# Optimization experiments

Measured on AMD Instinct MI355X. Metric: run time of the kernel, lower is better.

## Reference

```python
import jax, jax.numpy as jnp
import numpy as np

NUM_CLASSES = 10
HIDDEN = 64
_LABEL2MASK_THRESHOL = 500


def setup_inputs() -> dict:
    key = jax.random.key(0)
    ks = jax.random.split(key, 5)
    B, h, w = 4, 60, 80
    feature1 = jax.random.normal(ks[0], (B, 512, h, w), jnp.float32)
    feature2 = jax.random.normal(ks[1], (B, 512, h // 2, w // 2), jnp.float32)
    # kaiming_normal (fan_in, relu): std = sqrt(2 / fan_in)
    w1 = jax.random.normal(ks[2], (HIDDEN, 512), jnp.float32) * np.sqrt(2.0 / 512)
    w2 = jax.random.normal(ks[3], (HIDDEN, 512), jnp.float32) * np.sqrt(2.0 / 512)
    wc = jax.random.normal(ks[4], (NUM_CLASSES + 1, HIDDEN), jnp.float32) * np.sqrt(2.0 / HIDDEN)
    b1 = jnp.zeros((HIDDEN,), jnp.float32)
    b2 = jnp.zeros((HIDDEN,), jnp.float32)
    bc = jnp.zeros((NUM_CLASSES + 1,), jnp.float32)
    return {"feature1": feature1, "feature2": feature2, "w1": w1, "b1": b1,
            "w2": w2, "b2": b2, "wc": wc, "bc": bc}


def _conv1x1(x, w, b):
    # x: (B,C,H,W), w: (O,C), b: (O,)
    return jnp.einsum('bchw,oc->bohw', x, w) + b[None, :, None, None]


def _resize2x(x, s):
    B, C, H, W = x.shape
    # torch nn.Upsample(mode='bilinear', align_corners=False) == half-pixel bilinear
    return jax.image.resize(x, (B, C, H * s, W * s), method='bilinear')


def _label2bbx(seg, num_classes, thresh):
    # seg: (B,H,W) int. Fixed-shape, fully vectorized version of the nested
    # python-loop bbox extraction. Rows with pixel count < thresh are -1.
    B, H, W = seg.shape
    cls = jnp.arange(1, num_classes, dtype=seg.dtype)        # skip background cls 0
    mask = seg[:, None, :, :] == cls[None, :, None, None]    # (B,K,H,W)
    cnt = mask.sum(axis=(2, 3))
    xs = jnp.arange(W, dtype=jnp.int32)[None, None, None, :]
    ys = jnp.arange(H, dtype=jnp.int32)[None, None, :, None]
    x1 = jnp.min(jnp.where(mask, xs, W), axis=(2, 3))
    x2 = jnp.max(jnp.where(mask, xs, -1), axis=(2, 3))
    y1 = jnp.min(jnp.where(mask, ys, H), axis=(2, 3))
    y2 = jnp.max(jnp.where(mask, ys, -1), axis=(2, 3))
    K = num_classes - 1
    bid = jnp.broadcast_to(jnp.arange(B, dtype=jnp.int32)[:, None], (B, K))
    cid = jnp.broadcast_to(cls.astype(jnp.int32)[None, :], (B, K))
    rows = jnp.stack([bid, x1.astype(jnp.int32), y1.astype(jnp.int32),
                      x2.astype(jnp.int32), y2.astype(jnp.int32), cid], axis=-1)  # (B,K,6)
    valid = (cnt >= thresh)[..., None]
    rows = jnp.where(valid, rows, -1)
    return rows.reshape(B * K, 6)


def reference(feature1, feature2, w1, b1, w2, b2, wc, bc):
    f1 = jax.nn.relu(_conv1x1(feature1, w1, b1))
    f2 = jax.nn.relu(_conv1x1(feature2, w2, b2))
    f2 = _resize2x(f2, 2)
    feat = _resize2x(f1 + f2, 8)              # (B,64,480,640)
    logits = _conv1x1(feat, wc, bc)           # (B,11,480,640)
    probability = jax.nn.softmax(logits, axis=1)
    segmentation = jnp.argmax(probability, axis=1)
    bbx = _label2bbx(segmentation, NUM_CLASSES, _LABEL2MASK_THRESHOL)
    return probability, segmentation, bbx
```

## Files before the change

kernel.cpp:

```cpp
#include <hip/hip_runtime.h>

#define BN 4
#define CIN 512
#define H1 60
#define W1 80
#define P1 4800
#define H2 30
#define W2 40
#define P2 1200
#define HID 64
#define NCLS 11
#define HF 480
#define WF 640
#define PF 307200
#define THRESH 500

#define WT1_OFF 0
#define WT2_OFF 32768
#define F2_OFF  65536
#define PART_OFF F2_OFF
#define L_OFF   (65536 + 307200)
#define PP_OFF  603136

__device__ __forceinline__ void dma16(const float* g, float* l) {
    __builtin_amdgcn_global_load_lds(
        (const __attribute__((address_space(1))) void*)g,
        (__attribute__((address_space(3))) void*)l, 16, 0, 0);
}

__global__ void k0_init(const float* __restrict__ w1, const float* __restrict__ w2,
                        float* __restrict__ ws) {
    int idx = blockIdx.x * 256 + threadIdx.x;
    if (idx < 32768) {
        int c = idx >> 6, o = idx & 63;
        ws[WT1_OFF + idx] = w1[o * CIN + c];
    } else {
        int j = idx - 32768;
        int c = j >> 6, o = j & 63;
        ws[WT2_OFF + j] = w2[o * CIN + c];
    }
}

__global__ __launch_bounds__(256, 4) void k1_conv2(const float* __restrict__ x,
                                                   const float* __restrict__ b2,
                                                   float* __restrict__ ws) {
    __shared__ float lds[8320];
    const float* wt = ws + WT2_OFF;
    float* f2o = ws + F2_OFF;
    int blk = blockIdx.x;
    int b = blk / 150, tile = blk % 150;
    int t = threadIdx.x;
    int l = t & 63, w = t >> 6;
    int q = t & 1, og = (t >> 1) & 7, ch = t >> 4;
    int o0 = og * 8;
    int p0 = tile * 8;
    const float* xb = x + (size_t)b * CIN * P2 + p0;

    auto stage = [&](int s) {
        int buf = s & 1;
#pragma unroll
        for (int j = 0; j < 2; ++j) {
            int r0 = j * 128 + w * 32;
            int r  = r0 + (l >> 1);
            int cg = (r >> 4) * 32 + s * 16 + (r & 15);
            dma16(xb + (size_t)cg * P2 + (l & 1) * 4,
                  lds + buf * 2048 + r0 * 8);
        }
    };

    float acc[4][8];
#pragma unroll
    for (int j = 0; j < 4; ++j)
#pragma unroll
        for (int i = 0; i < 8; ++i) acc[j][i] = 0.f;

    stage(0);
    __syncthreads();
    const float* wp = wt + (ch * 32) * HID + o0;
    for (int s = 0; s < 2; ++s) {
        if (s < 1) stage(s + 1);
        const float* xs = lds + (s & 1) * 2048 + ch * 128 + q * 4;
#pragma unroll 4
        for (int cc = 0; cc < 16; ++cc) {
            float4 xv = *(const float4*)(xs + cc * 8);
            const float* wr = wp + (s * 16 + cc) * HID;
            float4 wa = *(const float4*)(wr);
            float4 wb = *(const float4*)(wr + 4);
            float w8[8] = {wa.x, wa.y, wa.z, wa.w, wb.x, wb.y, wb.z, wb.w};
            float x4[4] = {xv.x, xv.y, xv.z, xv.w};
#pragma unroll
            for (int j = 0; j < 4; ++j)
#pragma unroll
                for (int i = 0; i < 8; ++i) acc[j][i] = fmaf(w8[i], x4[j], acc[j][i]);
        }
        __syncthreads();
    }
#pragma unroll
    for (int j = 0; j < 4; ++j)
#pragma unroll
        for (int i = 0; i < 8; ++i)
            lds[ch * 520 + (q * 4 + j) * 65 + o0 + i] = acc[j][i];
    __syncthreads();

    if (t < 64) {
        int px = t >> 3, oo = (t & 7) * 8;
        float v[8];
#pragma unroll
        for (int i = 0; i < 8; ++i) {
            float s = 0.f;
#pragma unroll
            for (int c = 0; c < 16; ++c) s += lds[c * 520 + px * 65 + oo + i];
            v[i] = fmaxf(s + b2[oo + i], 0.f);
        }
        float* outp = f2o + ((size_t)b * P2 + p0 + px) * HID + oo;
        *(float4*)outp = make_float4(v[0], v[1], v[2], v[3]);
        *(float4*)(outp + 4) = make_float4(v[4], v[5], v[6], v[7]);
    }
}

__global__ __launch_bounds__(256, 2) void k2a_conv1(const float* __restrict__ x,
                                                    float* __restrict__ ws) {
    __shared__ float lds[16384];
    const float* wtg = ws + WT1_OFF;
    float* pp = ws + PP_OFF;
    int blk = blockIdx.x;
    int b = blk / 300;
    int rem = blk - b * 300;
    int hb = rem / 150;
    int tile = rem - hb * 150;
    int t = threadIdx.x;
    int l = t & 63;
    int q = t & 7, og = (t >> 3) & 7, ch = t >> 6;
    int o0 = og * 8;
    int p0 = tile * 32;
    const float* xc = x + (size_t)b * CIN * P1 + (size_t)(hb * 256 + ch * 64) * P1
                    + p0 + q * 4;

    float4 xA[8], xB[8];
    auto loadg = [&](float4* xb, int g) {
        const float* p = xc + (size_t)g * (8 * P1);
#pragma unroll
        for (int i = 0; i < 8; ++i) xb[i] = *(const float4*)(p + (size_t)i * P1);
    };

    loadg(xA, 0);

    {
        const float* src = wtg + hb * 16384 + ch * 4096;
#pragma unroll
        for (int i = 0; i < 16; ++i)
            dma16(src + i * 256 + l * 4, lds + ch * 4096 + i * 256);
    }
    __syncthreads();

    float acc[4][8];
#pragma unroll
    for (int j = 0; j < 4; ++j)
#pragma unroll
        for (int i = 0; i < 8; ++i) acc[j][i] = 0.f;

    const float* wl = lds + ch * 4096 + o0;
    auto computeg = [&](const float4* xb, int g) {
        const float* wr0 = wl + g * 8 * 64;
#pragma unroll
        for (int i = 0; i < 8; ++i) {
            float4 wa  = *(const float4*)(wr0 + i * 64);
            float4 wb4 = *(const float4*)(wr0 + i * 64 + 4);
            float w8[8] = {wa.x, wa.y, wa.z, wa.w, wb4.x, wb4.y, wb4.z, wb4.w};
            float x4[4] = {xb[i].x, xb[i].y, xb[i].z, xb[i].w};
#pragma unroll
            for (int j = 0; j < 4; ++j)
#pragma unroll
                for (int i2 = 0; i2 < 8; ++i2) acc[j][i2] = fmaf(w8[i2], x4[j], acc[j][i2]);
        }
    };

#pragma unroll 1
    for (int g = 0; g < 8; g += 2) {
        loadg(xB, min(g + 1, 7));
        computeg(xA, g);
        loadg(xA, min(g + 2, 7));
        computeg(xB, g + 1);
    }

    __syncthreads();
#pragma unroll
    for (int j = 0; j < 4; ++j)
#pragma unroll
        for (int i = 0; i < 8; ++i)
            lds[ch * 2080 + (q * 4 + j) * 65 + o0 + i] = acc[j][i];
    __syncthreads();

    {
        int px = t >> 3;
        int oo = (t & 7) * 8;
        float v[8];
#pragma unroll
        for (int i = 0; i < 8; ++i) {
            int a = px * 65 + oo + i;
            v[i] = lds[a] + lds[2080 + a] + lds[2 * 2080 + a] + lds[3 * 2080 + a];
        }
        float* outp = pp + ((size_t)(b * 2 + hb) * P1 + p0 + px) * HID + oo;
        *(float4*)outp = make_float4(v[0], v[1], v[2], v[3]);
        *(float4*)(outp + 4) = make_float4(v[4], v[5], v[6], v[7]);
    }
}

__global__ __launch_bounds__(256) void k2b_reduce(const float* __restrict__ b1,
                                                  const float* __restrict__ wc,
                                                  const float* __restrict__ bc,
                                                  float* __restrict__ ws) {
    __shared__ float g[2080];
    const float* pp = ws + PP_OFF;
    const float* f2 = ws + F2_OFF;
    float* lout = ws + L_OFF;
    int blk = blockIdx.x;
    int b = blk / 150, tile = blk % 150;
    int t = threadIdx.x;
    int p0 = tile * 32;

    {
        int px = t >> 3;
        int oo = (t & 7) * 8;
        int p = p0 + px;
        const float* h0 = pp + ((size_t)(b * 2 + 0) * P1 + p) * HID + oo;
        const float* h1 = pp + ((size_t)(b * 2 + 1) * P1 + p) * HID + oo;
        float4 a0 = *(const float4*)h0;
        float4 a1 = *(const float4*)(h0 + 4);
        float4 c0 = *(const float4*)h1;
        float4 c1 = *(const float4*)(h1 + 4);
        float hs[8] = {a0.x + c0.x, a0.y + c0.y, a0.z + c0.z, a0.w + c0.w,
                       a1.x + c1.x, a1.y + c1.y, a1.z + c1.z, a1.w + c1.w};

        int y = p / W1, xq = p - y * W1;
        float sy = fmaf((float)y, 0.5f, -0.25f);
        float fy = floorf(sy);
        float ty = sy - fy;
        int y0 = max(0, min(H2 - 1, (int)fy));
        int y1 = max(0, min(H2 - 1, (int)fy + 1));
        float sx = fmaf((float)xq, 0.5f, -0.25f);
        float fx = floorf(sx);
        float tx = sx - fx;
        int x0 = max(0, min(W2 - 1, (int)fx));
        int x1 = max(0, min(W2 - 1, (int)fx + 1));
        float wy0 = 1.f - ty, wx0 = 1.f - tx;
        const float* f2b = f2 + (size_t)b * P2 * HID;
        const float* r00 = f2b + (y0 * W2 + x0) * HID + oo;
        const float* r01 = f2b + (y0 * W2 + x1) * HID + oo;
        const float* r10 = f2b + (y1 * W2 + x0) * HID + oo;
        const float* r11 = f2b + (y1 * W2 + x1) * HID + oo;
#pragma unroll
        for (int i = 0; i < 8; ++i) {
            float f1v = fmaxf(hs[i] + b1[oo + i], 0.f);
            float v0 = r00[i] * wx0 + r01[i] * tx;
            float v1 = r10[i] * wx0 + r11[i] * tx;
            g[px * 65 + oo + i] = f1v + (v0 * wy0 + v1 * ty);
        }
    }
    __syncthreads();

    {
        int px2 = t & 31;
        int kg = t >> 5;
        int k2i = (kg < 3) ? kg + 8 : 8;
        float l1 = bc[kg];
        float l2 = bc[k2i];
#pragma unroll 8
        for (int o = 0; o < HID; ++o) {
            float gv = g[px2 * 65 + o];
            l1 = fmaf(wc[kg * HID + o], gv, l1);
            l2 = fmaf(wc[k2i * HID + o], gv, l2);
        }
        float* lrow = lout + ((size_t)b * P1 + p0 + px2) * 12;
        lrow[kg] = l1;
        if (kg < 3) lrow[kg + 8] = l2;
        else if (kg == 3) lrow[11] = 0.f;
    }
}

__global__ __launch_bounds__(256) void k4_main(float* __restrict__ out,
                                               float* __restrict__ ws) {
    __shared__ int s_cnt[9], s_x0[9], s_y0[9], s_x1[9], s_y1[9];
    const float* l = ws + L_OFF;
    int* partb = (int*)(ws + PART_OFF);
    int t = threadIdx.x;
    if (t < 9) { s_cnt[t] = 0; s_x0[t] = WF; s_y0[t] = HF; s_x1[t] = -1; s_y1[t] = -1; }
    __syncthreads();

    int fl = blockIdx.x * 256 + t;
    int b = fl / PF;
    int r = fl - b * PF;
    int Y = r / WF;
    int X = r - Y * WF;

    float sy = fmaf((float)Y, 0.125f, -0.4375f);
    float fy = floorf(sy);
    float ty = sy - fy;
    int y0 = max(0, min(H1 - 1, (int)fy));
    int y1 = max(0, min(H1 - 1, (int)fy + 1));
    float sx = fmaf((float)X, 0.125f, -0.4375f);
    float fx = floorf(sx);
    float tx = sx - fx;
    int x0 = max(0, min(W1 - 1, (int)fx));
    int x1 = max(0, min(W1 - 1, (int)fx + 1));
    float wy0 = 1.f - ty, wx0 = 1.f - tx;

    const float* lb = l + (size_t)b * P1 * 12;
    const float4* q00 = (const float4*)(lb + (y0 * W1 + x0) * 12);
    const float4* q01 = (const float4*)(lb + (y0 * W1 + x1) * 12);
    const float4* q10 = (const float4*)(lb + (y1 * W1 + x0) * 12);
    const float4* q11 = (const float4*)(lb + (y1 * W1 + x1) * 12);
    float l00[12], l01[12], l10[12], l11[12];
#pragma unroll
    for (int j = 0; j < 3; ++j) {
        ((float4*)l00)[j] = q00[j];
        ((float4*)l01)[j] = q01[j];
        ((float4*)l10)[j] = q10[j];
        ((float4*)l11)[j] = q11[j];
    }
    float li[11];
#pragma unroll
    for (int k = 0; k < 11; ++k) {
        float v0 = l00[k] * wx0 + l01[k] * tx;
        float v1 = l10[k] * wx0 + l11[k] * tx;
        li[k] = v0 * wy0 + v1 * ty;
    }
    int am = 0;
    float bm = li[0];
#pragma unroll
    for (int k = 1; k < 11; ++k) {
        if (li[k] > bm) { bm = li[k]; am = k; }
    }
    float e[11];
    float s = 0.f;
#pragma unroll
    for (int k = 0; k < 11; ++k) { e[k] = __expf(li[k] - bm); s += e[k]; }
    float rs = 1.f / s;
    size_t ob = (size_t)b * NCLS * PF + r;
#pragma unroll
    for (int k = 0; k < 11; ++k) out[ob + (size_t)k * PF] = e[k] * rs;
    out[(size_t)BN * NCLS * PF + fl] = (float)am;

    int lane = t & 63;
    int X0 = X & ~63;
    for (int c = 1; c <= 9; ++c) {
        unsigned long long m = __ballot(am == c);
        if (m != 0ULL && lane == 0) {
            int ci = c - 1;
            atomicAdd(&s_cnt[ci], (int)__popcll(m));
            atomicMin(&s_x0[ci], X0 + __builtin_ctzll(m));
            atomicMax(&s_x1[ci], X0 + 63 - __builtin_clzll(m));
            atomicMin(&s_y0[ci], Y);
            atomicMax(&s_y1[ci], Y);
        }
    }
    __syncthreads();
    if (t < 9) {
        int* pr = partb + blockIdx.x * 45 + t * 5;
        pr[0] = s_cnt[t];
        pr[1] = s_x0[t];
        pr[2] = s_y0[t];
        pr[3] = s_x1[t];
        pr[4] = s_y1[t];
    }
}

__global__ void k5_bbx(float* __restrict__ out, const float* __restrict__ ws) {
    const int* partb = (const int*)(ws + PART_OFF);
    int b = blockIdx.x / 9, c = blockIdx.x % 9;
    int t = threadIdx.x;
    int cnt = 0, mnx = WF, mny = HF, mxx = -1, mxy = -1;
    for (int i = t; i < 1200; i += 64) {
        const int* pr = partb + (size_t)(b * 1200 + i) * 45 + c * 5;
        cnt += pr[0];
        mnx = min(mnx, pr[1]);
        mny = min(mny, pr[2]);
        mxx = max(mxx, pr[3]);
        mxy = max(mxy, pr[4]);
    }
    for (int sft = 32; sft; sft >>= 1) {
        cnt += __shfl_xor(cnt, sft);
        mnx = min(mnx, __shfl_xor(mnx, sft));
        mny = min(mny, __shfl_xor(mny, sft));
        mxx = max(mxx, __shfl_xor(mxx, sft));
        mxy = max(mxy, __shfl_xor(mxy, sft));
    }
    if (t == 0) {
        float* row = out + (size_t)BN * NCLS * PF + (size_t)BN * PF + (size_t)(b * 9 + c) * 6;
        bool ok = cnt >= THRESH;
        row[0] = ok ? (float)b : -1.f;
        row[1] = ok ? (float)mnx : -1.f;
        row[2] = ok ? (float)mny : -1.f;
        row[3] = ok ? (float)mxx : -1.f;
        row[4] = ok ? (float)mxy : -1.f;
        row[5] = ok ? (float)(c + 1) : -1.f;
    }
}

extern "C" void kernel_launch(void* const* d_in, const int* in_sizes, int n_in,
                              void* d_out, int out_size, void* d_ws, size_t ws_size,
                              hipStream_t stream) {
    const float* f1 = (const float*)d_in[0];
    const float* f2 = (const float*)d_in[1];
    const float* w1 = (const float*)d_in[2];
    const float* b1 = (const float*)d_in[3];
    const float* w2 = (const float*)d_in[4];
    const float* b2 = (const float*)d_in[5];
    const float* wc = (const float*)d_in[6];
    const float* bc = (const float*)d_in[7];
    float* out = (float*)d_out;
    float* ws = (float*)d_ws;

    k0_init<<<dim3(256), dim3(256), 0, stream>>>(w1, w2, ws);
    k1_conv2<<<dim3(600), dim3(256), 0, stream>>>(f2, b2, ws);
    k2a_conv1<<<dim3(1200), dim3(256), 0, stream>>>(f1, ws);
    k2b_reduce<<<dim3(600), dim3(256), 0, stream>>>(b1, wc, bc, ws);
    k4_main<<<dim3(4800), dim3(256), 0, stream>>>(out, ws);
    k5_bbx<<<dim3(36), dim3(64), 0, stream>>>(out, ws);
}
```

Baseline: 167.3 us.

## Stage low-res logit rows in LDS per output row and add sched barriers

The upsample/softmax kernel now runs one 640-thread block per output row. It stages the two needed low-res logit rows into shared memory and reads the bilinear corners from LDS rather than from scattered global loads, so per-block partial bbox records drop from 1200 to 480 per image and the reduction kernel is adjusted to match. Separately, sched_barrier calls are inserted in the conv1 kernel to keep its load/compute software pipeline ordered. The price is a larger block, which can limit occupancy, plus an extra sync per block.

```diff
diff --git a/kernel.cpp b/kernel.cpp
--- a/kernel.cpp
+++ b/kernel.cpp
@@ -144,6 +144,7 @@
     };
 
     loadg(xA, 0);
+    __builtin_amdgcn_sched_barrier(0);
 
     {
         const float* src = wtg + hb * 16384 + ch * 4096;
@@ -178,8 +179,10 @@
 #pragma unroll 1
     for (int g = 0; g < 8; g += 2) {
         loadg(xB, min(g + 1, 7));
+        __builtin_amdgcn_sched_barrier(0);
         computeg(xA, g);
         loadg(xA, min(g + 2, 7));
+        __builtin_amdgcn_sched_barrier(0);
         computeg(xB, g + 1);
     }
 
@@ -278,38 +281,45 @@
     }
 }
 
-__global__ __launch_bounds__(256) void k4_main(float* __restrict__ out,
+__global__ __launch_bounds__(640) void k4_main(float* __restrict__ out,
                                                float* __restrict__ ws) {
+    __shared__ float sl[1920];
     __shared__ int s_cnt[9], s_x0[9], s_y0[9], s_x1[9], s_y1[9];
     const float* l = ws + L_OFF;
     int* partb = (int*)(ws + PART_OFF);
     int t = threadIdx.x;
     if (t < 9) { s_cnt[t] = 0; s_x0[t] = WF; s_y0[t] = HF; s_x1[t] = -1; s_y1[t] = -1; }
-    __syncthreads();
-
-    int fl = blockIdx.x * 256 + t;
-    int b = fl / PF;
-    int r = fl - b * PF;
-    int Y = r / WF;
-    int X = r - Y * WF;
+
+    int blk = blockIdx.x;
+    int b = blk / HF;
+    int Y = blk - b * HF;
 
     float sy = fmaf((float)Y, 0.125f, -0.4375f);
     float fy = floorf(sy);
     float ty = sy - fy;
     int y0 = max(0, min(H1 - 1, (int)fy));
     int y1 = max(0, min(H1 - 1, (int)fy + 1));
+    float wy0 = 1.f - ty;
+
+    const float* lb = l + (size_t)b * P1 * 12;
+    const float* row0 = lb + y0 * W1 * 12;
+    const float* row1 = lb + y1 * W1 * 12;
+    for (int i = t; i < 960; i += 640) sl[i] = row0[i];
+    for (int i = t; i < 960; i += 640) sl[960 + i] = row1[i];
+    __syncthreads();
+
+    int X = t;
     float sx = fmaf((float)X, 0.125f, -0.4375f);
     float fx = floorf(sx);
     float tx = sx - fx;
     int x0 = max(0, min(W1 - 1, (int)fx));
     int x1 = max(0, min(W1 - 1, (int)fx + 1));
-    float wy0 = 1.f - ty, wx0 = 1.f - tx;
-
-    const float* lb = l + (size_t)b * P1 * 12;
-    const float4* q00 = (const float4*)(lb + (y0 * W1 + x0) * 12);
-    const float4* q01 = (const float4*)(lb + (y0 * W1 + x1) * 12);
-    const float4* q10 = (const float4*)(lb + (y1 * W1 + x0) * 12);
-    const float4* q11 = (const float4*)(lb + (y1 * W1 + x1) * 12);
+    float wx0 = 1.f - tx;
+
+    const float4* q00 = (const float4*)(sl + x0 * 12);
+    const float4* q01 = (const float4*)(sl + x1 * 12);
+    const float4* q10 = (const float4*)(sl + 960 + x0 * 12);
+    const float4* q11 = (const float4*)(sl + 960 + x1 * 12);
     float l00[12], l01[12], l10[12], l11[12];
 #pragma unroll
     for (int j = 0; j < 3; ++j) {
@@ -336,10 +346,11 @@
 #pragma unroll
     for (int k = 0; k < 11; ++k) { e[k] = __expf(li[k] - bm); s += e[k]; }
     float rs = 1.f / s;
+    int r = Y * WF + X;
     size_t ob = (size_t)b * NCLS * PF + r;
 #pragma unroll
     for (int k = 0; k < 11; ++k) out[ob + (size_t)k * PF] = e[k] * rs;
-    out[(size_t)BN * NCLS * PF + fl] = (float)am;
+    out[(size_t)BN * NCLS * PF + (size_t)b * PF + r] = (float)am;
 
     int lane = t & 63;
     int X0 = X & ~63;
@@ -356,7 +367,7 @@
     }
     __syncthreads();
     if (t < 9) {
-        int* pr = partb + blockIdx.x * 45 + t * 5;
+        int* pr = partb + blk * 45 + t * 5;
         pr[0] = s_cnt[t];
         pr[1] = s_x0[t];
         pr[2] = s_y0[t];
@@ -370,8 +381,8 @@
     int b = blockIdx.x / 9, c = blockIdx.x % 9;
     int t = threadIdx.x;
     int cnt = 0, mnx = WF, mny = HF, mxx = -1, mxy = -1;
-    for (int i = t; i < 1200; i += 64) {
-        const int* pr = partb + (size_t)(b * 1200 + i) * 45 + c * 5;
+    for (int i = t; i < HF; i += 64) {
+        const int* pr = partb + (size_t)(b * HF + i) * 45 + c * 5;
         cnt += pr[0];
         mnx = min(mnx, pr[1]);
         mny = min(mny, pr[2]);
@@ -415,6 +426,6 @@
     k1_conv2<<<dim3(600), dim3(256), 0, stream>>>(f2, b2, ws);
     k2a_conv1<<<dim3(1200), dim3(256), 0, stream>>>(f1, ws);
     k2b_reduce<<<dim3(600), dim3(256), 0, stream>>>(b1, wc, bc, ws);
-    k4_main<<<dim3(4800), dim3(256), 0, stream>>>(out, ws);
+    k4_main<<<dim3(1920), dim3(640), 0, stream>>>(out, ws);
     k5_bbx<<<dim3(36), dim3(64), 0, stream>>>(out, ws);
 }
```

After: 171.8 us. 1.03x slower.
